# Performance work log

Hardware: AMD Instinct MI355X
Metric: run time of the kernel (lower is better)

The kernel has to match this reference:

```python
import jax, jax.numpy as jnp
import numpy as np

D_MODEL = 2048
N_HEADS = 16
N_KV = 4
D_K = D_MODEL // N_HEADS  # 128
B, T = 2, 2048


def setup_inputs() -> dict:
    key = jax.random.key(0)
    ks = jax.random.split(key, 10)
    s = 1.0 / np.sqrt(D_MODEL)
    x = jax.random.normal(ks[0], (B, T, D_MODEL), dtype=jnp.float32)
    mask = jnp.ones((B, 1, T, T), dtype=bool)
    Wq = jax.random.uniform(ks[1], (D_MODEL, D_MODEL), minval=-s, maxval=s, dtype=jnp.float32)
    bq = jax.random.uniform(ks[2], (D_MODEL,), minval=-s, maxval=s, dtype=jnp.float32)
    Wk = jax.random.uniform(ks[3], (D_MODEL, N_KV * D_K), minval=-s, maxval=s, dtype=jnp.float32)
    bk = jax.random.uniform(ks[4], (N_KV * D_K,), minval=-s, maxval=s, dtype=jnp.float32)
    Wv = jax.random.uniform(ks[5], (D_MODEL, N_KV * D_K), minval=-s, maxval=s, dtype=jnp.float32)
    bv = jax.random.uniform(ks[6], (N_KV * D_K,), minval=-s, maxval=s, dtype=jnp.float32)
    Wo = jax.random.uniform(ks[7], (D_MODEL, D_MODEL), minval=-s, maxval=s, dtype=jnp.float32)
    bo = jax.random.uniform(ks[8], (D_MODEL,), minval=-s, maxval=s, dtype=jnp.float32)
    return {"x": x, "mask": mask, "Wq": Wq, "bq": bq, "Wk": Wk, "bk": bk,
            "Wv": Wv, "bv": bv, "Wo": Wo, "bo": bo}


def reference(x, mask, Wq, bq, Wk, bk, Wv, bv, Wo, bo):
    Bn, Tn, _ = x.shape
    g = N_HEADS // N_KV
    # projections
    q = (x @ Wq + bq).reshape(Bn, Tn, N_HEADS, D_K).transpose(0, 2, 1, 3)  # [B,H,T,d]
    k = (x @ Wk + bk).reshape(Bn, Tn, N_KV, D_K).transpose(0, 2, 1, 3)     # [B,Hk,T,d]
    v = (x @ Wv + bv).reshape(Bn, Tn, N_KV, D_K).transpose(0, 2, 1, 3)
    # GQA broadcast: group Q heads as [B,Hk,g,T,d]; no repeat_interleave copy
    qg = q.reshape(Bn, N_KV, g, Tn, D_K)
    scores = jnp.einsum('bkgqd,bkld->bkgql', qg, k) / jnp.sqrt(jnp.float32(D_K))
    scores = jnp.where(mask[:, :, None, :, :], scores, jnp.float32(-1e9))
    attn = jax.nn.softmax(scores, axis=-1)  # dropout=0 (eval)
    out = jnp.einsum('bkgql,bkld->bkgqd', attn, v)  # [B,Hk,g,T,d]
    out = out.reshape(Bn, N_HEADS, Tn, D_K).transpose(0, 2, 1, 3).reshape(Bn, Tn, D_MODEL)
    return out @ Wo + bo
```

## Files before the change

kernel.cpp:

```cpp
#include <hip/hip_runtime.h>
#include <hip/hip_bf16.h>

typedef __attribute__((ext_vector_type(8))) short short8;
typedef __attribute__((ext_vector_type(4))) float f32x4;
typedef __attribute__((ext_vector_type(16))) float f32x16;
typedef __attribute__((ext_vector_type(2))) unsigned uint2v;

__device__ __forceinline__ unsigned short f2bf(float f) {
  union { float f; unsigned u; } v; v.f = f;
  unsigned u = v.u;
  return (unsigned short)((u + 0x7fffu + ((u >> 16) & 1u)) >> 16);
}

__device__ __forceinline__ unsigned packbf2(float a, float b) {
  union { __hip_bfloat162 h; unsigned u; } c;
  c.h = __float22bfloat162_rn(float2{a, b});
  return c.u;
}

__device__ __forceinline__ void gload16(void* lds, const void* g) {
  __builtin_amdgcn_global_load_lds(
      (__attribute__((address_space(1))) unsigned int*)g,
      (__attribute__((address_space(3))) unsigned int*)lds, 16, 0, 0);
}

#define BAR() asm volatile("s_barrier" ::: "memory")
#define LGKM0() asm volatile("s_waitcnt lgkmcnt(0)" ::: "memory")

__global__ void prep(const float* __restrict__ x, const float* __restrict__ Wq,
                     const float* __restrict__ Wk, const float* __restrict__ Wv,
                     const float* __restrict__ Wo,
                     unsigned short* __restrict__ xb,
                     unsigned short* __restrict__ wqkvT,
                     unsigned short* __restrict__ woT) {
  int id = blockIdx.x, tid = threadIdx.x;
  if (id < 4096) {
    int i = id * 256 + tid;
    const float4* p = (const float4*)x + (size_t)i * 2;
    float4 a = p[0], b = p[1];
    union { unsigned short u[8]; short8 v; } o;
    o.u[0] = f2bf(a.x); o.u[1] = f2bf(a.y); o.u[2] = f2bf(a.z); o.u[3] = f2bf(a.w);
    o.u[4] = f2bf(b.x); o.u[5] = f2bf(b.y); o.u[6] = f2bf(b.z); o.u[7] = f2bf(b.w);
    *(short8*)(xb + (size_t)i * 8) = o.v;
    return;
  }
  __shared__ float tile[32][33];
  const float* src; unsigned short* dst; int N, rowOff, tn, tk;
  if (id < 8192)       { int t = id - 4096;  src = Wq; dst = wqkvT; N = 2048; rowOff = 0;    tn = t & 63; tk = t >> 6; }
  else if (id < 9216)  { int t = id - 8192;  src = Wk; dst = wqkvT; N = 512;  rowOff = 2048; tn = t & 15; tk = t >> 4; }
  else if (id < 10240) { int t = id - 9216;  src = Wv; dst = wqkvT; N = 512;  rowOff = 2560; tn = t & 15; tk = t >> 4; }
  else                 { int t = id - 10240; src = Wo; dst = woT;   N = 2048; rowOff = 0;    tn = t & 63; tk = t >> 6; }
  int n0 = tn * 32, k0 = tk * 32;
  int c = tid & 31, rr = tid >> 5;
#pragma unroll
  for (int p = 0; p < 4; ++p) {
    int r = p * 8 + rr;
    tile[r][c] = src[(size_t)(k0 + r) * N + n0 + c];
  }
  __syncthreads();
#pragma unroll
  for (int p = 0; p < 4; ++p) {
    int r = p * 8 + rr;
    dst[(size_t)(rowOff + n0 + r) * 2048 + k0 + c] = f2bf(tile[c][r]);
  }
}

__global__ __launch_bounds__(512, 4) void gemm64(
    const unsigned short* __restrict__ A, const unsigned short* __restrict__ Bt,
    int K,
    const float* __restrict__ b0, const float* __restrict__ b1,
    const float* __restrict__ b2,
    unsigned short* __restrict__ oq, unsigned short* __restrict__ ok,
    unsigned short* __restrict__ ov) {
  __shared__ char L[81920];
  int tid = threadIdx.x, wid = tid >> 6, lane = tid & 63, lo = lane & 15, hi = lane >> 4;
  int wr = wid >> 2, wc = wid & 3;
  int m0 = blockIdx.x * 64, n0 = blockIdx.y * 256;
  const char* Ab = (const char*)A + (size_t)m0 * K * 2;
  const char* Bb = (const char*)Bt + (size_t)n0 * K * 2;
  f32x4 acc[2][4] = {};
  int NT = K >> 6;

  auto SA = [&](int p, int kt, int c) {
    int o = c * 1024 + lane * 16;
    int r = o >> 7;
    int cb = (o & 127) ^ ((r & 7) << 4);
    gload16(L + p * 40960 + c * 1024, Ab + (size_t)r * K * 2 + kt * 128 + cb);
  };
  auto SB = [&](int p, int kt, int c) {
    int o = c * 1024 + lane * 16;
    int r = o >> 7;
    int cb = (o & 127) ^ ((r & 7) << 4);
    gload16(L + p * 40960 + 8192 + c * 1024, Bb + (size_t)r * K * 2 + kt * 128 + cb);
  };
  int ev0 = (wid & 3) + (wid >> 2) * 8, ev1 = 16 + ev0;
  int od0 = 4 + (wid & 3) + (wid >> 2) * 8, od1 = 16 + od0;

  SA(0, 0, wid);
  SB(0, 0, ev0); SB(0, 0, ev1); SB(0, 0, od0); SB(0, 0, od1);
  SA(1, 1, wid); SB(1, 1, ev0); SB(1, 1, ev1);
  asm volatile("s_waitcnt vmcnt(3)" ::: "memory");
  BAR();

  for (int t = 0; t < NT; ++t) {
    int p = t & 1;
    const char* AB = L + p * 40960;
    const char* BB = AB + 8192;
    short8 af[2][2], bf0[2][2], bf1[2][2];

#pragma unroll
    for (int ks = 0; ks < 2; ++ks) {
#pragma unroll
      for (int i = 0; i < 2; ++i) {
        int row = wr * 32 + i * 16 + lo;
        af[ks][i] = *(const short8*)(AB + ((row * 128 + ks * 64 + hi * 16) ^ ((row & 7) << 4)));
      }
#pragma unroll
      for (int j = 0; j < 2; ++j) {
        int row = wc * 64 + j * 16 + lo;
        bf0[ks][j] = *(const short8*)(BB + ((row * 128 + ks * 64 + hi * 16) ^ ((row & 7) << 4)));
      }
    }
    if (t + 1 < NT) { SB(p ^ 1, t + 1, od0); SB(p ^ 1, t + 1, od1); }
    BAR(); LGKM0();
    __builtin_amdgcn_s_setprio(1);
#pragma unroll
    for (int ks = 0; ks < 2; ++ks)
#pragma unroll
      for (int i = 0; i < 2; ++i)
#pragma unroll
        for (int j = 0; j < 2; ++j)
          acc[i][j] = __builtin_amdgcn_mfma_f32_16x16x32_bf16(af[ks][i], bf0[ks][j], acc[i][j], 0, 0, 0);
    __builtin_amdgcn_s_setprio(0);
    if (t >= NT - 3) { asm volatile("s_waitcnt vmcnt(0)" ::: "memory"); }
    else             { asm volatile("s_waitcnt vmcnt(5)" ::: "memory"); }
    BAR();

#pragma unroll
    for (int ks = 0; ks < 2; ++ks)
#pragma unroll
      for (int j = 0; j < 2; ++j) {
        int row = wc * 64 + 32 + j * 16 + lo;
        bf1[ks][j] = *(const short8*)(BB + ((row * 128 + ks * 64 + hi * 16) ^ ((row & 7) << 4)));
      }
    if (t + 2 < NT) { SA(p, t + 2, wid); SB(p, t + 2, ev0); SB(p, t + 2, ev1); }
    BAR(); LGKM0();
    __builtin_amdgcn_s_setprio(1);
#pragma unroll
    for (int ks = 0; ks < 2; ++ks)
#pragma unroll
      for (int i = 0; i < 2; ++i)
#pragma unroll
        for (int j = 0; j < 2; ++j)
          acc[i][2 + j] = __builtin_amdgcn_mfma_f32_16x16x32_bf16(af[ks][i], bf1[ks][j], acc[i][2 + j], 0, 0, 0);
    __builtin_amdgcn_s_setprio(0);
    if (t >= NT - 3) { asm volatile("s_waitcnt vmcnt(0)" ::: "memory"); }
    else             { asm volatile("s_waitcnt vmcnt(5)" ::: "memory"); }
    BAR();
  }

#pragma unroll
  for (int ii = 0; ii < 2; ++ii) {
    int mbase = m0 + wr * 32 + ii * 16 + hi * 4;
#pragma unroll
    for (int jj = 0; jj < 4; ++jj) {
      int n = n0 + wc * 64 + jj * 16 + lo;
      float bias;
      if (n < 2048) bias = b0[n];
      else if (n < 2560) bias = b1[n - 2048];
      else bias = b2[n - 2560];
#pragma unroll
      for (int r = 0; r < 4; ++r) {
        int mm = mbase + r;
        int b = mm >> 11, t = mm & 2047;
        float val = acc[ii][jj][r] + bias;
        if (n < 2048) {
          int h = n >> 7, d = n & 127;
          oq[(((size_t)(b * 16 + h)) * 2048 + t) * 128 + d] =
              f2bf(val * (0.08838834764831845f * 1.4426950408889634f));
        } else if (n < 2560) {
          int kvh = (n - 2048) >> 7, d = (n - 2048) & 127;
          ok[(((size_t)(b * 4 + kvh)) * 2048 + t) * 128 + d] = f2bf(val);
        } else {
          int kvh = (n - 2560) >> 7, d = (n - 2560) & 127;
          ov[(((size_t)(b * 4 + kvh)) * 128 + d) * 2048 + t] = f2bf(val);
        }
      }
    }
  }
}

__global__ __launch_bounds__(512, 2) void gemmO(
    const unsigned short* __restrict__ A, const unsigned short* __restrict__ Bt,
    int K, const float* __restrict__ bias, float* __restrict__ of) {
  __shared__ char L[98304];
  int tid = threadIdx.x, wid = tid >> 6, lane = tid & 63, lo = lane & 15, hi = lane >> 4;
  int wr = wid >> 2, wc = wid & 3;
  int m0 = blockIdx.x * 128, n0 = blockIdx.y * 256;
  const char* Ab = (const char*)A + (size_t)m0 * K * 2;
  const char* Bb = (const char*)Bt + (size_t)n0 * K * 2;
  f32x4 acc[4][4] = {};
  int NT = K >> 6;

  auto SA = [&](int p, int kt, int c) {
    int o = c * 1024 + lane * 16;
    int r = o >> 7;
    int cb = (o & 127) ^ ((r & 7) << 4);
    gload16(L + p * 49152 + c * 1024, Ab + (size_t)r * K * 2 + kt * 128 + cb);
  };
  auto SB = [&](int p, int kt, int c) {
    int o = c * 1024 + lane * 16;
    int r = o >> 7;
    int cb = (o & 127) ^ ((r & 7) << 4);
    gload16(L + p * 49152 + 16384 + c * 1024, Bb + (size_t)r * K * 2 + kt * 128 + cb);
  };
  int ev0 = (wid & 3) + (wid >> 2) * 8, ev1 = 16 + ev0;
  int od0 = 4 + (wid & 3) + (wid >> 2) * 8, od1 = 16 + od0;

  SA(0, 0, 2 * wid); SA(0, 0, 2 * wid + 1);
  SB(0, 0, ev0); SB(0, 0, ev1); SB(0, 0, od0); SB(0, 0, od1);
  SA(1, 1, 2 * wid); SA(1, 1, 2 * wid + 1); SB(1, 1, ev0); SB(1, 1, ev1);
  asm volatile("s_waitcnt vmcnt(4)" ::: "memory");
  BAR();

  for (int t = 0; t < NT; ++t) {
    int p = t & 1;
    const char* AB = L + p * 49152;
    const char* BB = AB + 16384;
    short8 af[2][4], bf0[2][2], bf1[2][2];

#pragma unroll
    for (int ks = 0; ks < 2; ++ks) {
#pragma unroll
      for (int i = 0; i < 4; ++i) {
        int row = wr * 64 + i * 16 + lo;
        af[ks][i] = *(const short8*)(AB + ((row * 128 + ks * 64 + hi * 16) ^ ((row & 7) << 4)));
      }
#pragma unroll
      for (int j = 0; j < 2; ++j) {
        int row = wc * 64 + j * 16 + lo;
        bf0[ks][j] = *(const short8*)(BB + ((row * 128 + ks * 64 + hi * 16) ^ ((row & 7) << 4)));
      }
    }
    if (t + 1 < NT) { SB(p ^ 1, t + 1, od0); SB(p ^ 1, t + 1, od1); }
    BAR(); LGKM0();
    __builtin_amdgcn_s_setprio(1);
#pragma unroll
    for (int ks = 0; ks < 2; ++ks)
#pragma unroll
      for (int i = 0; i < 4; ++i)
#pragma unroll
        for (int j = 0; j < 2; ++j)
          acc[i][j] = __builtin_amdgcn_mfma_f32_16x16x32_bf16(af[ks][i], bf0[ks][j], acc[i][j], 0, 0, 0);
    __builtin_amdgcn_s_setprio(0);
    if (t >= NT - 3) { asm volatile("s_waitcnt vmcnt(0)" ::: "memory"); }
    else             { asm volatile("s_waitcnt vmcnt(6)" ::: "memory"); }
    BAR();

#pragma unroll
    for (int ks = 0; ks < 2; ++ks)
#pragma unroll
      for (int j = 0; j < 2; ++j) {
        int row = wc * 64 + 32 + j * 16 + lo;
        bf1[ks][j] = *(const short8*)(BB + ((row * 128 + ks * 64 + hi * 16) ^ ((row & 7) << 4)));
      }
    if (t + 2 < NT) {
      SA(p, t + 2, 2 * wid); SA(p, t + 2, 2 * wid + 1);
      SB(p, t + 2, ev0); SB(p, t + 2, ev1);
    }
    BAR(); LGKM0();
    __builtin_amdgcn_s_setprio(1);
#pragma unroll
    for (int ks = 0; ks < 2; ++ks)
#pragma unroll
      for (int i = 0; i < 4; ++i)
#pragma unroll
        for (int j = 0; j < 2; ++j)
          acc[i][2 + j] = __builtin_amdgcn_mfma_f32_16x16x32_bf16(af[ks][i], bf1[ks][j], acc[i][2 + j], 0, 0, 0);
    __builtin_amdgcn_s_setprio(0);
    if (t >= NT - 3) { asm volatile("s_waitcnt vmcnt(0)" ::: "memory"); }
    else             { asm volatile("s_waitcnt vmcnt(6)" ::: "memory"); }
    BAR();
  }

#pragma unroll
  for (int ii = 0; ii < 4; ++ii) {
    int mbase = m0 + wr * 64 + ii * 16 + hi * 4;
#pragma unroll
    for (int jj = 0; jj < 4; ++jj) {
      int n = n0 + wc * 64 + jj * 16 + lo;
      float bv = bias[n];
#pragma unroll
      for (int r = 0; r < 4; ++r)
        of[(size_t)(mbase + r) * 2048 + n] = acc[ii][jj][r] + bv;
    }
  }
}

__device__ __forceinline__ void stageK(char* KLb, const char* kcb, int w, int lane, int t0) {
#pragma unroll
  for (int j = 0; j < 4; ++j) {
    int o = j * 4096 + w * 1024 + lane * 16;
    int row = o >> 8, col = o & 255;
    gload16(KLb + j * 4096 + w * 1024,
            kcb + (size_t)(t0 + row) * 256 + (col ^ ((row & 15) << 4)));
  }
}
__device__ __forceinline__ void stageV(char* VLb, const char* vcb, int w, int lane, int t0) {
#pragma unroll
  for (int j = 0; j < 4; ++j) {
    int o = j * 4096 + w * 1024 + lane * 16;
    int d = o >> 7, col = o & 127;
    gload16(VLb + j * 4096 + w * 1024,
            vcb + (size_t)d * 4096 + t0 * 2 + (col ^ ((d & 7) << 4)));
  }
}

__global__ __launch_bounds__(256, 2) void attn_fwd(
    const unsigned short* __restrict__ q, const unsigned short* __restrict__ kg,
    const unsigned short* __restrict__ vtg, unsigned short* __restrict__ attn) {
  __shared__ unsigned short kbuf[8192];
  __shared__ unsigned short vbuf[8192];
  int tid = threadIdx.x, w = tid >> 6, lane = tid & 63;
  int l31 = lane & 31, hi5 = lane >> 5;
  int tq0 = blockIdx.x * 128, h = blockIdx.y, b = blockIdx.z, kvh = h >> 2;
  int qrow = tq0 + w * 32;

  const unsigned short* qbase = q + ((size_t)(b * 16 + h)) * 2048 * 128;
  short8 qf[8];
#pragma unroll
  for (int ds_ = 0; ds_ < 8; ++ds_)
    qf[ds_] = *(const short8*)(qbase + (size_t)(qrow + l31) * 128 + ds_ * 16 + hi5 * 8);

  f32x16 oacc[4] = {};
  f32x16 lacc = {};
  float mrow = -1e30f;
  const short8 onesv = {16256, 16256, 16256, 16256, 16256, 16256, 16256, 16256};

  const char* kcb = (const char*)(kg + ((size_t)(b * 4 + kvh)) * 2048 * 128);
  const char* vcb = (const char*)(vtg + ((size_t)(b * 4 + kvh)) * 128 * 2048);
  char* KL = (char*)kbuf;
  char* VL = (char*)vbuf;

  for (int t0 = 0; t0 < 2048; t0 += 64) {
    stageK(KL, kcb, w, lane, t0);
    stageV(VL, vcb, w, lane, t0);
    asm volatile("s_waitcnt vmcnt(0)" ::: "memory");
    BAR();

    f32x16 s[2] = {};
    __builtin_amdgcn_s_setprio(1);
#pragma unroll
    for (int ds_ = 0; ds_ < 8; ++ds_) {
#pragma unroll
      for (int f = 0; f < 2; ++f) {
        int row = f * 32 + l31;
        short8 kf = *(const short8*)(KL + ((row * 256 + ds_ * 32 + hi5 * 16) ^ ((row & 15) << 4)));
        s[f] = __builtin_amdgcn_mfma_f32_32x32x16_bf16(kf, qf[ds_], s[f], 0, 0, 0);
      }
    }
    __builtin_amdgcn_s_setprio(0);

    float am = fmaxf(s[0][0], s[0][1]);
#pragma unroll
    for (int r = 2; r < 14; r += 2) am = fmaxf(fmaxf(am, s[0][r]), s[0][r + 1]);
    am = fmaxf(fmaxf(am, s[0][14]), s[0][15]);
#pragma unroll
    for (int r = 0; r < 16; r += 2) am = fmaxf(fmaxf(am, s[1][r]), s[1][r + 1]);

    if (!__all(am <= mrow + 8.f)) {
      float ar = fmaxf(am, __shfl_xor(am, 32));
      float mnew = fmaxf(mrow, ar);
      float fsv = __builtin_amdgcn_exp2f(mrow - mnew);
      mrow = mnew;
#pragma unroll
      for (int g = 0; g < 4; ++g)
#pragma unroll
        for (int r = 0; r < 4; ++r) {
          float fsr = __shfl(fsv, r + 8 * g + 4 * hi5);
          lacc[4 * g + r] *= fsr;
#pragma unroll
          for (int db = 0; db < 4; ++db) oacc[db][4 * g + r] *= fsr;
        }
    }

    unsigned pk01[2][4], pk23[2][4];
#pragma unroll
    for (int f = 0; f < 2; ++f)
#pragma unroll
      for (int g = 0; g < 4; ++g) {
        float p0 = __builtin_amdgcn_exp2f(s[f][4 * g + 0] - mrow);
        float p1 = __builtin_amdgcn_exp2f(s[f][4 * g + 1] - mrow);
        float p2 = __builtin_amdgcn_exp2f(s[f][4 * g + 2] - mrow);
        float p3 = __builtin_amdgcn_exp2f(s[f][4 * g + 3] - mrow);
        pk01[f][g] = packbf2(p0, p1);
        pk23[f][g] = packbf2(p2, p3);
      }

    short8 pA[4];
#pragma unroll
    for (int f = 0; f < 2; ++f)
#pragma unroll
      for (int p = 0; p < 2; ++p) {
        uint2v a01 = __builtin_amdgcn_permlane32_swap(pk01[f][2 * p], pk01[f][2 * p + 1], false, false);
        uint2v a23 = __builtin_amdgcn_permlane32_swap(pk23[f][2 * p], pk23[f][2 * p + 1], false, false);
        union { unsigned u[4]; short8 v; } pa;
        pa.u[0] = a01.x; pa.u[1] = a23.x; pa.u[2] = a01.y; pa.u[3] = a23.y;
        pA[2 * f + p] = pa.v;
      }

    __builtin_amdgcn_s_setprio(1);
#pragma unroll
    for (int db = 0; db < 4; ++db) {
      int d = db * 32 + l31;
      int sw = (d & 7) << 4;
#pragma unroll
      for (int step = 0; step < 4; ++step) {
        short8 vf = *(const short8*)(VL + ((d * 128 + step * 32 + hi5 * 16) ^ sw));
        oacc[db] = __builtin_amdgcn_mfma_f32_32x32x16_bf16(pA[step], vf, oacc[db], 0, 0, 0);
      }
    }
#pragma unroll
    for (int step = 0; step < 4; ++step)
      lacc = __builtin_amdgcn_mfma_f32_32x32x16_bf16(pA[step], onesv, lacc, 0, 0, 0);
    __builtin_amdgcn_s_setprio(0);
    LGKM0();
    BAR();
  }

  unsigned short* ob = attn + ((size_t)b * 2048) * 2048 + h * 128;
#pragma unroll
  for (int g = 0; g < 4; ++g)
#pragma unroll
    for (int r = 0; r < 4; ++r) {
      float lr = 1.0f / lacc[4 * g + r];
      int t = qrow + r + 8 * g + 4 * hi5;
#pragma unroll
      for (int db = 0; db < 4; ++db)
        ob[(size_t)t * 2048 + db * 32 + l31] = f2bf(oacc[db][4 * g + r] * lr);
    }
}

extern "C" void kernel_launch(void* const* d_in, const int* in_sizes, int n_in,
                              void* d_out, int out_size, void* d_ws, size_t ws_size,
                              hipStream_t stream) {
  const float* x  = (const float*)d_in[0];
  const float* Wq = (const float*)d_in[2];
  const float* bq = (const float*)d_in[3];
  const float* Wk = (const float*)d_in[4];
  const float* bk = (const float*)d_in[5];
  const float* Wv = (const float*)d_in[6];
  const float* bv = (const float*)d_in[7];
  const float* Wo = (const float*)d_in[8];
  const float* bo = (const float*)d_in[9];
  float* out = (float*)d_out;

  char* ws = (char*)d_ws;
  unsigned short* xb    = (unsigned short*)(ws);
  unsigned short* wqkvT = (unsigned short*)(ws + 16777216);
  unsigned short* woT   = (unsigned short*)(ws + 29360128);
  unsigned short* qb    = (unsigned short*)(ws + 37748736);
  unsigned short* kbw   = (unsigned short*)(ws + 54525952);
  unsigned short* vtw   = (unsigned short*)(ws + 58720256);
  unsigned short* attnb = (unsigned short*)(ws + 62914560);

  prep<<<dim3(14336), dim3(256), 0, stream>>>(x, Wq, Wk, Wv, Wo, xb, wqkvT, woT);

  gemm64<<<dim3(64, 12), dim3(512), 0, stream>>>(
      xb, wqkvT, 2048, bq, bk, bv, qb, kbw, vtw);

  attn_fwd<<<dim3(16, 16, 2), dim3(256), 0, stream>>>(qb, kbw, vtw, attnb);

  gemmO<<<dim3(32, 8), dim3(512), 0, stream>>>(attnb, woT, 2048, bo, out);
}
```

Before: 207.3 us.

## Split attention KV range across two wave groups and merge partial softmax in LDS

The attention block doubles to 512 threads. Two halves each process half of the key/value sequence for the same 128 query rows, using separate LDS staging buffers. At the end, half 1 writes its unnormalized output, row max and row sum to LDS, and half 0 rescales and merges them before the bf16 store. This doubles the waves working on each query tile so that, with only 512 blocks, the per-block serial loop is shorter and latency is hidden better. The cost is a larger LDS footprint (about 65 KB per block), which may cut the number of resident blocks, plus a merge step.

```diff
diff --git a/kernel.cpp b/kernel.cpp
--- a/kernel.cpp
+++ b/kernel.cpp
@@ -297,34 +297,34 @@
   }
 }
 
-__device__ __forceinline__ void stageK(char* KLb, const char* kcb, int w, int lane, int t0) {
+__device__ __forceinline__ void stageK(char* KLb, const char* kcb, int wl, int lane, int t0) {
 #pragma unroll
   for (int j = 0; j < 4; ++j) {
-    int o = j * 4096 + w * 1024 + lane * 16;
+    int o = j * 4096 + wl * 1024 + lane * 16;
     int row = o >> 8, col = o & 255;
-    gload16(KLb + j * 4096 + w * 1024,
+    gload16(KLb + j * 4096 + wl * 1024,
             kcb + (size_t)(t0 + row) * 256 + (col ^ ((row & 15) << 4)));
   }
 }
-__device__ __forceinline__ void stageV(char* VLb, const char* vcb, int w, int lane, int t0) {
+__device__ __forceinline__ void stageV(char* VLb, const char* vcb, int wl, int lane, int t0) {
 #pragma unroll
   for (int j = 0; j < 4; ++j) {
-    int o = j * 4096 + w * 1024 + lane * 16;
+    int o = j * 4096 + wl * 1024 + lane * 16;
     int d = o >> 7, col = o & 127;
-    gload16(VLb + j * 4096 + w * 1024,
+    gload16(VLb + j * 4096 + wl * 1024,
             vcb + (size_t)d * 4096 + t0 * 2 + (col ^ ((d & 7) << 4)));
   }
 }
 
-__global__ __launch_bounds__(256, 2) void attn_fwd(
+__global__ __launch_bounds__(512, 2) void attn_fwd(
     const unsigned short* __restrict__ q, const unsigned short* __restrict__ kg,
     const unsigned short* __restrict__ vtg, unsigned short* __restrict__ attn) {
-  __shared__ unsigned short kbuf[8192];
-  __shared__ unsigned short vbuf[8192];
+  __shared__ char L[66560];
   int tid = threadIdx.x, w = tid >> 6, lane = tid & 63;
+  int wl = w & 3, half = w >> 2;
   int l31 = lane & 31, hi5 = lane >> 5;
   int tq0 = blockIdx.x * 128, h = blockIdx.y, b = blockIdx.z, kvh = h >> 2;
-  int qrow = tq0 + w * 32;
+  int qrow = tq0 + wl * 32;
 
   const unsigned short* qbase = q + ((size_t)(b * 16 + h)) * 2048 * 128;
   short8 qf[8];
@@ -339,12 +339,13 @@
 
   const char* kcb = (const char*)(kg + ((size_t)(b * 4 + kvh)) * 2048 * 128);
   const char* vcb = (const char*)(vtg + ((size_t)(b * 4 + kvh)) * 128 * 2048);
-  char* KL = (char*)kbuf;
-  char* VL = (char*)vbuf;
-
-  for (int t0 = 0; t0 < 2048; t0 += 64) {
-    stageK(KL, kcb, w, lane, t0);
-    stageV(VL, vcb, w, lane, t0);
+  char* KL = L + half * 32768;
+  char* VL = KL + 16384;
+
+  for (int t0 = 0; t0 < 1024; t0 += 64) {
+    int tg = half * 1024 + t0;
+    stageK(KL, kcb, wl, lane, tg);
+    stageV(VL, vcb, wl, lane, tg);
     asm volatile("s_waitcnt vmcnt(0)" ::: "memory");
     BAR();
 
@@ -428,17 +429,47 @@
     BAR();
   }
 
-  unsigned short* ob = attn + ((size_t)b * 2048) * 2048 + h * 128;
-#pragma unroll
-  for (int g = 0; g < 4; ++g)
-#pragma unroll
-    for (int r = 0; r < 4; ++r) {
-      float lr = 1.0f / lacc[4 * g + r];
-      int t = qrow + r + 8 * g + 4 * hi5;
-#pragma unroll
-      for (int db = 0; db < 4; ++db)
-        ob[(size_t)t * 2048 + db * 32 + l31] = f2bf(oacc[db][4 * g + r] * lr);
-    }
+  float* Ox = (float*)L;
+  float* lm = (float*)(L + 65536);
+  if (half == 1) {
+#pragma unroll
+    for (int g = 0; g < 4; ++g)
+#pragma unroll
+      for (int r = 0; r < 4; ++r) {
+        int row = r + 8 * g + 4 * hi5;
+#pragma unroll
+        for (int db = 0; db < 4; ++db)
+          Ox[((wl * 32) + row) * 128 + db * 32 + l31] = oacc[db][4 * g + r];
+        if (l31 == 0) lm[(wl * 2 + 1) * 32 + row] = lacc[4 * g + r];
+      }
+    if (hi5 == 0) lm[(wl * 2 + 0) * 32 + l31] = mrow;
+  }
+  __syncthreads();
+  if (half == 0) {
+    unsigned short* ob = attn + ((size_t)b * 2048) * 2048 + h * 128;
+    float mB = lm[(wl * 2 + 0) * 32 + l31];
+    float mN = fmaxf(mrow, mB);
+    float fA = __builtin_amdgcn_exp2f(mrow - mN);
+    float fB = __builtin_amdgcn_exp2f(mB - mN);
+#pragma unroll
+    for (int g = 0; g < 4; ++g)
+#pragma unroll
+      for (int r = 0; r < 4; ++r) {
+        int row = r + 8 * g + 4 * hi5;
+        float fAr = __shfl(fA, row);
+        float fBr = __shfl(fB, row);
+        float lB = lm[(wl * 2 + 1) * 32 + row];
+        float lN = lacc[4 * g + r] * fAr + lB * fBr;
+        float inv = 1.0f / lN;
+        int t = qrow + row;
+#pragma unroll
+        for (int db = 0; db < 4; ++db) {
+          float oB = Ox[((wl * 32) + row) * 128 + db * 32 + l31];
+          ob[(size_t)t * 2048 + db * 32 + l31] =
+              f2bf((oacc[db][4 * g + r] * fAr + oB * fBr) * inv);
+        }
+      }
+  }
 }
 
 extern "C" void kernel_launch(void* const* d_in, const int* in_sizes, int n_in,
@@ -469,7 +500,7 @@
   gemm64<<<dim3(64, 12), dim3(512), 0, stream>>>(
       xb, wqkvT, 2048, bq, bk, bv, qb, kbw, vtw);
 
-  attn_fwd<<<dim3(16, 16, 2), dim3(256), 0, stream>>>(qb, kbw, vtw, attnb);
+  attn_fwd<<<dim3(16, 16, 2), dim3(512), 0, stream>>>(qb, kbw, vtw, attnb);
 
   gemmO<<<dim3(32, 8), dim3(512), 0, stream>>>(attnb, woT, 2048, bo, out);
 }
```

New measurement: 224.2 us. 8.1% more time.

## Split attention KV range into two halves with a separate merge kernel

Applied to the files above, without the earlier changes.

Splits the key/value sequence of attention across two blocks per query tile (flash-decoding style split-K), doubling the grid from 512 to 1024 blocks to fill more CUs on the MI355X. Each half writes its unnormalized bf16 output plus running max and sum, and a new merge kernel rescales and combines the halves into the attention buffer. This adds an extra launch, extra global traffic for the partial outputs, and an extra bf16 rounding of the partials. It also reuses the xb workspace as scratch for one partial.

```diff
diff --git a/kernel.cpp b/kernel.cpp
--- a/kernel.cpp
+++ b/kernel.cpp
@@ -10,6 +10,11 @@
   union { float f; unsigned u; } v; v.f = f;
   unsigned u = v.u;
   return (unsigned short)((u + 0x7fffu + ((u >> 16) & 1u)) >> 16);
+}
+
+__device__ __forceinline__ float bf2f(unsigned short us) {
+  union { unsigned u; float f; } v; v.u = ((unsigned)us) << 16;
+  return v.f;
 }
 
 __device__ __forceinline__ unsigned packbf2(float a, float b) {
@@ -318,12 +323,16 @@
 
 __global__ __launch_bounds__(256, 2) void attn_fwd(
     const unsigned short* __restrict__ q, const unsigned short* __restrict__ kg,
-    const unsigned short* __restrict__ vtg, unsigned short* __restrict__ attn) {
+    const unsigned short* __restrict__ vtg,
+    unsigned short* __restrict__ op0, unsigned short* __restrict__ op1,
+    float2* __restrict__ lm) {
   __shared__ unsigned short kbuf[8192];
   __shared__ unsigned short vbuf[8192];
   int tid = threadIdx.x, w = tid >> 6, lane = tid & 63;
   int l31 = lane & 31, hi5 = lane >> 5;
-  int tq0 = blockIdx.x * 128, h = blockIdx.y, b = blockIdx.z, kvh = h >> 2;
+  int tq0 = blockIdx.x * 128, h = blockIdx.y;
+  int b = blockIdx.z >> 1, half = blockIdx.z & 1;
+  int kvh = h >> 2;
   int qrow = tq0 + w * 32;
 
   const unsigned short* qbase = q + ((size_t)(b * 16 + h)) * 2048 * 128;
@@ -342,9 +351,10 @@
   char* KL = (char*)kbuf;
   char* VL = (char*)vbuf;
 
-  for (int t0 = 0; t0 < 2048; t0 += 64) {
-    stageK(KL, kcb, w, lane, t0);
-    stageV(VL, vcb, w, lane, t0);
+  for (int t0 = 0; t0 < 1024; t0 += 64) {
+    int tg = half * 1024 + t0;
+    stageK(KL, kcb, w, lane, tg);
+    stageV(VL, vcb, w, lane, tg);
     asm volatile("s_waitcnt vmcnt(0)" ::: "memory");
     BAR();
 
@@ -428,17 +438,45 @@
     BAR();
   }
 
-  unsigned short* ob = attn + ((size_t)b * 2048) * 2048 + h * 128;
+  unsigned short* op = (half ? op1 : op0) +
+                       (((size_t)(b * 16 + h)) * 2048 + qrow) * 128;
+  float2* lmw = lm + ((size_t)(half * 2 + b) * 16 + h) * 2048 + qrow;
 #pragma unroll
   for (int g = 0; g < 4; ++g)
 #pragma unroll
     for (int r = 0; r < 4; ++r) {
-      float lr = 1.0f / lacc[4 * g + r];
-      int t = qrow + r + 8 * g + 4 * hi5;
+      int row = r + 8 * g + 4 * hi5;
 #pragma unroll
       for (int db = 0; db < 4; ++db)
-        ob[(size_t)t * 2048 + db * 32 + l31] = f2bf(oacc[db][4 * g + r] * lr);
-    }
+        op[(size_t)row * 128 + db * 32 + l31] = f2bf(oacc[db][4 * g + r]);
+      float mr = __shfl(mrow, row);
+      if (l31 == 0) lmw[row] = float2{mr, lacc[4 * g + r]};
+    }
+}
+
+__global__ void attn_merge(const unsigned short* __restrict__ o0,
+                           const unsigned short* __restrict__ o1,
+                           const float2* __restrict__ lm,
+                           unsigned short* __restrict__ attnb) {
+  int gid = blockIdx.x * 256 + threadIdx.x;
+  int d8 = gid & 15;
+  int t  = (gid >> 4) & 2047;
+  int h  = (gid >> 15) & 15;
+  int b  = gid >> 19;
+  size_t rowi = ((size_t)(b * 16 + h)) * 2048 + t;
+  float2 A = lm[rowi], B = lm[rowi + 65536];
+  float mN = fmaxf(A.x, B.x);
+  float f0 = __builtin_amdgcn_exp2f(A.x - mN);
+  float f1 = __builtin_amdgcn_exp2f(B.x - mN);
+  float inv = 1.0f / (A.y * f0 + B.y * f1);
+  f0 *= inv; f1 *= inv;
+  short8 v0 = *(const short8*)(o0 + rowi * 128 + d8 * 8);
+  short8 v1 = *(const short8*)(o1 + rowi * 128 + d8 * 8);
+  union { unsigned short u[8]; short8 v; } o;
+#pragma unroll
+  for (int j = 0; j < 8; ++j)
+    o.u[j] = f2bf(bf2f((unsigned short)v0[j]) * f0 + bf2f((unsigned short)v1[j]) * f1);
+  *(short8*)(attnb + ((size_t)b * 2048 + t) * 2048 + h * 128 + d8 * 8) = o.v;
 }
 
 extern "C" void kernel_launch(void* const* d_in, const int* in_sizes, int n_in,
@@ -463,13 +501,16 @@
   unsigned short* kbw   = (unsigned short*)(ws + 54525952);
   unsigned short* vtw   = (unsigned short*)(ws + 58720256);
   unsigned short* attnb = (unsigned short*)(ws + 62914560);
+  unsigned short* op1   = (unsigned short*)(ws + 79691776);
+  float2*         lmb   = (float2*)(ws + 96468992);
 
   prep<<<dim3(14336), dim3(256), 0, stream>>>(x, Wq, Wk, Wv, Wo, xb, wqkvT, woT);
 
   gemm64<<<dim3(64, 12), dim3(512), 0, stream>>>(
       xb, wqkvT, 2048, bq, bk, bv, qb, kbw, vtw);
 
-  attn_fwd<<<dim3(16, 16, 2), dim3(256), 0, stream>>>(qb, kbw, vtw, attnb);
+  attn_fwd<<<dim3(16, 16, 4), dim3(256), 0, stream>>>(qb, kbw, vtw, xb, op1, lmb);
+  attn_merge<<<dim3(4096), dim3(256), 0, stream>>>(xb, op1, lmb, attnb);
 
   gemmO<<<dim3(32, 8), dim3(512), 0, stream>>>(attnb, woT, 2048, bo, out);
 }
```

New measurement: 219.5 us. 5.9% more time.

## Double-buffer K/V tiles and software-pipeline QK^T one tile ahead

Applied to the files above, without the earlier changes.

Attention kernel now double-buffers K and V tiles in LDS and issues the global loads for tile t+2 while tile t is being processed. QK^T for the next tile is computed before the softmax and PV of the current tile, so MFMA work overlaps the exp/softmax phase. The aim is to hide global-load latency and the serialized load-then-compute barrier of each iteration. LDS use doubles to 64KB per block, which may reduce occupancy below the 2 blocks per CU requested by launch bounds. Holding two score sets raises register pressure.

```diff
diff --git a/kernel.cpp b/kernel.cpp
--- a/kernel.cpp
+++ b/kernel.cpp
@@ -319,8 +319,8 @@
 __global__ __launch_bounds__(256, 2) void attn_fwd(
     const unsigned short* __restrict__ q, const unsigned short* __restrict__ kg,
     const unsigned short* __restrict__ vtg, unsigned short* __restrict__ attn) {
-  __shared__ unsigned short kbuf[8192];
-  __shared__ unsigned short vbuf[8192];
+  __shared__ unsigned short kbuf[16384];
+  __shared__ unsigned short vbuf[16384];
   int tid = threadIdx.x, w = tid >> 6, lane = tid & 63;
   int l31 = lane & 31, hi5 = lane >> 5;
   int tq0 = blockIdx.x * 128, h = blockIdx.y, b = blockIdx.z, kvh = h >> 2;
@@ -342,31 +342,53 @@
   char* KL = (char*)kbuf;
   char* VL = (char*)vbuf;
 
-  for (int t0 = 0; t0 < 2048; t0 += 64) {
-    stageK(KL, kcb, w, lane, t0);
-    stageV(VL, vcb, w, lane, t0);
-    asm volatile("s_waitcnt vmcnt(0)" ::: "memory");
-    BAR();
-
-    f32x16 s[2] = {};
+  auto QKT = [&](const char* KB, f32x16 (&s)[2]) {
+    s[0] = f32x16{}; s[1] = f32x16{};
     __builtin_amdgcn_s_setprio(1);
 #pragma unroll
     for (int ds_ = 0; ds_ < 8; ++ds_) {
 #pragma unroll
       for (int f = 0; f < 2; ++f) {
         int row = f * 32 + l31;
-        short8 kf = *(const short8*)(KL + ((row * 256 + ds_ * 32 + hi5 * 16) ^ ((row & 15) << 4)));
+        short8 kf = *(const short8*)(KB + ((row * 256 + ds_ * 32 + hi5 * 16) ^ ((row & 15) << 4)));
         s[f] = __builtin_amdgcn_mfma_f32_32x32x16_bf16(kf, qf[ds_], s[f], 0, 0, 0);
       }
     }
     __builtin_amdgcn_s_setprio(0);
-
-    float am = fmaxf(s[0][0], s[0][1]);
-#pragma unroll
-    for (int r = 2; r < 14; r += 2) am = fmaxf(fmaxf(am, s[0][r]), s[0][r + 1]);
-    am = fmaxf(fmaxf(am, s[0][14]), s[0][15]);
-#pragma unroll
-    for (int r = 0; r < 16; r += 2) am = fmaxf(fmaxf(am, s[1][r]), s[1][r + 1]);
+  };
+
+  f32x16 s0[2], s1[2];
+
+  stageK(KL, kcb, w, lane, 0);
+  stageV(VL, vcb, w, lane, 0);
+  stageK(KL + 16384, kcb, w, lane, 64);
+  asm volatile("s_waitcnt vmcnt(4)" ::: "memory");
+  BAR();
+  QKT(KL, s0);
+  stageV(VL + 16384, vcb, w, lane, 64);
+  LGKM0();
+  BAR();
+
+  auto body = [&](int t, f32x16 (&cur)[2], f32x16 (&nxt)[2]) {
+    int p = t & 1;
+    char* Kp = KL + p * 16384;
+    char* Kq = KL + (p ^ 1) * 16384;
+    char* Vp = VL + p * 16384;
+
+    if (t + 2 < 32) stageK(Kp, kcb, w, lane, (t + 2) * 64);
+    if (t + 2 < 32)      { asm volatile("s_waitcnt vmcnt(8)" ::: "memory"); }
+    else if (t + 1 < 32) { asm volatile("s_waitcnt vmcnt(4)" ::: "memory"); }
+    else                 { asm volatile("s_waitcnt vmcnt(0)" ::: "memory"); }
+    BAR();
+
+    if (t + 1 < 32) QKT(Kq, nxt);
+
+    float am = fmaxf(cur[0][0], cur[0][1]);
+#pragma unroll
+    for (int r = 2; r < 14; r += 2) am = fmaxf(fmaxf(am, cur[0][r]), cur[0][r + 1]);
+    am = fmaxf(fmaxf(am, cur[0][14]), cur[0][15]);
+#pragma unroll
+    for (int r = 0; r < 16; r += 2) am = fmaxf(fmaxf(am, cur[1][r]), cur[1][r + 1]);
 
     if (!__all(am <= mrow + 8.f)) {
       float ar = fmaxf(am, __shfl_xor(am, 32));
@@ -389,10 +411,10 @@
     for (int f = 0; f < 2; ++f)
 #pragma unroll
       for (int g = 0; g < 4; ++g) {
-        float p0 = __builtin_amdgcn_exp2f(s[f][4 * g + 0] - mrow);
-        float p1 = __builtin_amdgcn_exp2f(s[f][4 * g + 1] - mrow);
-        float p2 = __builtin_amdgcn_exp2f(s[f][4 * g + 2] - mrow);
-        float p3 = __builtin_amdgcn_exp2f(s[f][4 * g + 3] - mrow);
+        float p0 = __builtin_amdgcn_exp2f(cur[f][4 * g + 0] - mrow);
+        float p1 = __builtin_amdgcn_exp2f(cur[f][4 * g + 1] - mrow);
+        float p2 = __builtin_amdgcn_exp2f(cur[f][4 * g + 2] - mrow);
+        float p3 = __builtin_amdgcn_exp2f(cur[f][4 * g + 3] - mrow);
         pk01[f][g] = packbf2(p0, p1);
         pk23[f][g] = packbf2(p2, p3);
       }
@@ -401,12 +423,12 @@
 #pragma unroll
     for (int f = 0; f < 2; ++f)
 #pragma unroll
-      for (int p = 0; p < 2; ++p) {
-        uint2v a01 = __builtin_amdgcn_permlane32_swap(pk01[f][2 * p], pk01[f][2 * p + 1], false, false);
-        uint2v a23 = __builtin_amdgcn_permlane32_swap(pk23[f][2 * p], pk23[f][2 * p + 1], false, false);
+      for (int pp = 0; pp < 2; ++pp) {
+        uint2v a01 = __builtin_amdgcn_permlane32_swap(pk01[f][2 * pp], pk01[f][2 * pp + 1], false, false);
+        uint2v a23 = __builtin_amdgcn_permlane32_swap(pk23[f][2 * pp], pk23[f][2 * pp + 1], false, false);
         union { unsigned u[4]; short8 v; } pa;
         pa.u[0] = a01.x; pa.u[1] = a23.x; pa.u[2] = a01.y; pa.u[3] = a23.y;
-        pA[2 * f + p] = pa.v;
+        pA[2 * f + pp] = pa.v;
       }
 
     __builtin_amdgcn_s_setprio(1);
@@ -416,7 +438,7 @@
       int sw = (d & 7) << 4;
 #pragma unroll
       for (int step = 0; step < 4; ++step) {
-        short8 vf = *(const short8*)(VL + ((d * 128 + step * 32 + hi5 * 16) ^ sw));
+        short8 vf = *(const short8*)(Vp + ((d * 128 + step * 32 + hi5 * 16) ^ sw));
         oacc[db] = __builtin_amdgcn_mfma_f32_32x32x16_bf16(pA[step], vf, oacc[db], 0, 0, 0);
       }
     }
@@ -426,6 +448,12 @@
     __builtin_amdgcn_s_setprio(0);
     LGKM0();
     BAR();
+    if (t + 2 < 32) stageV(Vp, vcb, w, lane, (t + 2) * 64);
+  };
+
+  for (int t = 0; t < 32; t += 2) {
+    body(t, s0, s1);
+    body(t + 1, s1, s0);
   }
 
   unsigned short* ob = attn + ((size_t)b * 2048) * 2048 + h * 128;
```

Result: no change. 208.3 us (+0.4%).
